# Optimization experiments

Measured on AMD Instinct MI355X. Metric: run time of the kernel, lower is better.

The kernel has to match this reference:

```python
import jax, jax.numpy as jnp
import numpy as np


def setup_inputs() -> dict:
    key = jax.random.key(0)
    k0, k1, k2, k3, k4 = jax.random.split(key, 5)
    B, S, D, H = 64, 512, 512, 512
    scale = 1.0 / np.sqrt(H)
    inp = {
        "input_features": jax.random.normal(k0, (B, S, D), dtype=jnp.float32),
        # PyTorch GRU params, gate order (r, z, n)
        "W_ih": jax.random.uniform(k1, (3 * H, D), jnp.float32, -scale, scale),
        "W_hh": jax.random.uniform(k2, (3 * H, H), jnp.float32, -scale, scale),
        "b_ih": jax.random.uniform(k3, (3 * H,), jnp.float32, -scale, scale),
        "b_hh": jax.random.uniform(k4, (3 * H,), jnp.float32, -scale, scale),
    }
    return inp


def reference(input_features, W_ih, W_hh, b_ih, b_hh):
    """1-layer unidirectional GRU with residual connection (input_dim == hidden_dim,
    so self.linear is Identity). Returns (residual_output [B,S,H],
    stacked per-step hidden [1,B,S,H]) matching the torch module."""
    B, S, D = input_features.shape
    H = W_hh.shape[1]

    # Precompute input projections for all timesteps in one GEMM: [B,S,3H]
    x_proj = jnp.einsum("bsd,gd->bsg", input_features, W_ih) + b_ih
    x_proj_t = jnp.transpose(x_proj, (1, 0, 2))  # [S,B,3H]

    def step(h, xp):
        # xp: [B,3H], h: [B,H]
        gh = h @ W_hh.T + b_hh  # [B,3H]
        r = jax.nn.sigmoid(xp[:, :H] + gh[:, :H])
        z = jax.nn.sigmoid(xp[:, H:2 * H] + gh[:, H:2 * H])
        n = jnp.tanh(xp[:, 2 * H:] + r * gh[:, 2 * H:])
        h_new = (1.0 - z) * n + z * h
        return h_new, h_new

    h0 = jnp.zeros((B, H), dtype=input_features.dtype)
    _, hs = jax.lax.scan(step, h0, x_proj_t)  # hs: [S,B,H]
    outputs = jnp.transpose(hs, (1, 0, 2))  # [B,S,H] raw GRU outputs

    residual_output = input_features + outputs  # Identity residual (D == H)
    hidden_stacked = outputs[None]  # [1,B,S,H]: per-step hidden of the single layer
    return residual_output, hidden_stacked
```

## Files before the change

### kernel.cpp

```cpp
#include <hip/hip_runtime.h>

typedef unsigned short u16;
typedef unsigned int   u32;
typedef unsigned long long u64;
typedef __attribute__((ext_vector_type(4))) float f32x4;
typedef __attribute__((ext_vector_type(8))) short s16x8;
typedef __attribute__((ext_vector_type(4))) unsigned short u16x4;
typedef __attribute__((ext_vector_type(8))) unsigned short u16x8;

__device__ __forceinline__ float bf2f(u16 u) {
    u32 i = ((u32)u) << 16;
    return __builtin_bit_cast(float, i);
}
__device__ __forceinline__ u16 f2bf(float f) {
    u32 i = __builtin_bit_cast(u32, f);
    u32 lsb = (i >> 16) & 1u;
    i += 0x7fffu + lsb;
    return (u16)(i >> 16);
}

__device__ __forceinline__ void ld_cc16(s16x8& r, const u16* p) {
    asm volatile("global_load_dwordx4 %0, %1, off sc0 sc1" : "=v"(r) : "v"(p));
}
__device__ __forceinline__ void st_cc8(u16* p, u64 v) {
    asm volatile("global_store_dwordx2 %0, %1, off sc0 sc1" :: "v"(p), "v"(v) : "memory");
}

__global__ __launch_bounds__(256) void prep(const float* __restrict__ Wih,
                                            const float* __restrict__ Whh,
                                            u16* __restrict__ Wihb,
                                            u16* __restrict__ Wfrag) {
    int id = blockIdx.x * 256 + threadIdx.x;
    {
        const float* s = Wih + (size_t)id * 8;
        f32x4 x0 = *(const f32x4*)s;
        f32x4 x1 = *(const f32x4*)(s + 4);
        u16x8 o;
        for (int j = 0; j < 4; ++j) { o[j] = f2bf(x0[j]); o[4 + j] = f2bf(x1[j]); }
        *(u16x8*)(Wihb + (size_t)id * 8) = o;
    }
    {
        int lane = id & 63;
        int ks   = (id >> 6) & 15;
        int wnt  = id >> 10;
        int nt   = wnt % 3;
        int w    = wnt / 3;
        int row  = nt * 512 + w * 16 + (lane & 15);
        int k    = ks * 32 + (lane >> 4) * 8;
        const float* s = Whh + (size_t)row * 512 + k;
        f32x4 x0 = *(const f32x4*)s;
        f32x4 x1 = *(const f32x4*)(s + 4);
        u16x8 o;
        for (int j = 0; j < 4; ++j) { o[j] = f2bf(x0[j]); o[4 + j] = f2bf(x1[j]); }
        *(u16x8*)(Wfrag + (size_t)id * 8) = o;
    }
}

__global__ __launch_bounds__(256) void gemm_xproj(const float* __restrict__ inp,
                                                  const u16* __restrict__ Wihb,
                                                  const float* __restrict__ bih,
                                                  u16* __restrict__ xp) {
    __shared__ u16 lA[128 * 64];
    __shared__ u16 lB[128 * 64];
    const int bid = blockIdx.x;
    const int mtile = bid & 255;
    const int ntile = bid >> 8;
    const int tid = threadIdx.x;
    const int l = tid & 63;
    const int wid = tid >> 6;
    const int s0 = mtile * 2;
    const int n0 = ntile * 128;

    f32x4 acc[4][4];
    for (int a = 0; a < 4; ++a)
        for (int b = 0; b < 4; ++b) acc[a][b] = (f32x4){0.f, 0.f, 0.f, 0.f};

    for (int k0 = 0; k0 < 512; k0 += 64) {
        if (k0) __syncthreads();
        for (int i = 0; i < 4; ++i) {
            int boff = (wid * 4 + i) * 1024 + l * 16;
            int r = boff >> 7;
            int kb = boff & 127;
            const char* src = (const char*)Wihb + (size_t)(n0 + r) * 1024 + (size_t)k0 * 2 + kb;
            __builtin_amdgcn_global_load_lds(
                (const __attribute__((address_space(1))) u32*)src,
                (__attribute__((address_space(3))) u32*)((char*)lB + (wid * 4 + i) * 1024),
                16, 0, 0);
        }
        for (int i = 0; i < 4; ++i) {
            int c = i * 256 + tid;
            int r = c >> 3;
            int ck = c & 7;
            int b = r & 63;
            int sl = r >> 6;
            const float* src = inp + ((size_t)(b * 512 + s0 + sl) * 512 + k0 + ck * 8);
            f32x4 x0 = *(const f32x4*)src;
            f32x4 x1 = *(const f32x4*)(src + 4);
            u16x8 o;
            for (int j = 0; j < 4; ++j) { o[j] = f2bf(x0[j]); o[4 + j] = f2bf(x1[j]); }
            *(u16x8*)(&lA[r * 64 + ck * 8]) = o;
        }
        __syncthreads();
        for (int kk = 0; kk < 2; ++kk) {
            s16x8 af[4], bf[4];
            for (int am = 0; am < 4; ++am)
                af[am] = *(const s16x8*)(&lA[((wid >> 1) * 64 + am * 16 + (l & 15)) * 64 + kk * 32 + (l >> 4) * 8]);
            for (int bn = 0; bn < 4; ++bn)
                bf[bn] = *(const s16x8*)(&lB[((wid & 1) * 64 + bn * 16 + (l & 15)) * 64 + kk * 32 + (l >> 4) * 8]);
            for (int am = 0; am < 4; ++am)
                for (int bn = 0; bn < 4; ++bn)
                    acc[am][bn] = __builtin_amdgcn_mfma_f32_16x16x32_bf16(af[am], bf[bn], acc[am][bn], 0, 0, 0);
        }
    }
    for (int am = 0; am < 4; ++am) {
        for (int bn = 0; bn < 4; ++bn) {
            int m_base = mtile * 128 + (wid >> 1) * 64 + am * 16;
            int row0 = m_base + ((l >> 4) << 2);
            int s = row0 >> 6;
            int b0 = row0 & 63;
            int n = n0 + (wid & 1) * 64 + bn * 16 + (l & 15);
            int g = n >> 9;
            int col = n & 511;
            int ww = col >> 4;
            int mt2 = b0 >> 4;
            size_t el = ((((size_t)s * 32 + ww) * 4 + mt2) * 3 + g) * 256 + l * 4;
            float bias = bih[n];
            u16x4 o;
            for (int j = 0; j < 4; ++j) o[j] = f2bf(acc[am][bn][j] + bias);
            *(u16x4*)(xp + el) = o;
        }
    }
}

__global__ __launch_bounds__(256, 1) void gru_scan(const u16* __restrict__ xp,
                                                   const u16* __restrict__ Wfrag,
                                                   const float* __restrict__ bhh,
                                                   const float* __restrict__ inp,
                                                   float* __restrict__ dout,
                                                   u16* __restrict__ hbuf,
                                                   int* __restrict__ cnt) {
    const int w = blockIdx.x;
    const int tid = threadIdx.x;
    const int l = tid & 63;
    const int mt = tid >> 6;
    float* out_res = dout;
    float* out_hid = dout + (size_t)64 * 512 * 512;

    __shared__ u16 tlds[4][16][20];

    const u16* wsrc = Wfrag + (size_t)w * 24576;
    s16x8 wreg[3][16];
#pragma unroll
    for (int g = 0; g < 3; ++g)
#pragma unroll
        for (int kk = 0; kk < 16; ++kk)
            wreg[g][kk] = *(const s16x8*)(wsrc + (size_t)(g * 16 + kk) * 512 + l * 8);

    const float bh0 = bhh[0 * 512 + w * 16 + (l & 15)];
    const float bh1 = bhh[1 * 512 + w * 16 + (l & 15)];
    const float bh2 = bhh[2 * 512 + w * 16 + (l & 15)];
    float hold[4] = {0.f, 0.f, 0.f, 0.f};
    const int bb = mt * 16 + ((l >> 4) << 2);
    const int c = w * 16 + (l & 15);

    s16x8 af[16];
#pragma unroll
    for (int kk = 0; kk < 16; ++kk) af[kk] = (s16x8){0, 0, 0, 0, 0, 0, 0, 0};

    const u16* xpp = xp + ((((size_t)0 * 32 + w) * 4 + mt) * 3) * 256 + l * 4;
    u16x4 xv0 = *(const u16x4*)(xpp);
    u16x4 xv1 = *(const u16x4*)(xpp + 256);
    u16x4 xv2 = *(const u16x4*)(xpp + 512);
    float inv[4];
#pragma unroll
    for (int j = 0; j < 4; ++j)
        inv[j] = inp[((size_t)(bb + j) * 512 + 0) * 512 + c];

    for (int t = 0; t < 512; ++t) {
        asm volatile("s_waitcnt vmcnt(0)" ::: "memory");
        __builtin_amdgcn_sched_barrier(0);

        f32x4 acc0 = (f32x4){0.f, 0.f, 0.f, 0.f};
        f32x4 acc1 = (f32x4){0.f, 0.f, 0.f, 0.f};
        f32x4 acc2 = (f32x4){0.f, 0.f, 0.f, 0.f};
#pragma unroll
        for (int kk = 0; kk < 16; ++kk) {
            acc0 = __builtin_amdgcn_mfma_f32_16x16x32_bf16(af[kk], wreg[0][kk], acc0, 0, 0, 0);
            acc1 = __builtin_amdgcn_mfma_f32_16x16x32_bf16(af[kk], wreg[1][kk], acc1, 0, 0, 0);
            acc2 = __builtin_amdgcn_mfma_f32_16x16x32_bf16(af[kk], wreg[2][kk], acc2, 0, 0, 0);
        }

        float hn[4];
#pragma unroll
        for (int j = 0; j < 4; ++j) {
            float xr = bf2f(xv0[j]), xz = bf2f(xv1[j]), xn = bf2f(xv2[j]);
            float rr = 1.f / (1.f + __expf(-(xr + acc0[j] + bh0)));
            float zz = 1.f / (1.f + __expf(-(xz + acc1[j] + bh1)));
            float nx = xn + rr * (acc2[j] + bh2);
            float e2 = __expf(-2.f * nx);
            float nn = (1.f - e2) / (1.f + e2);
            float h = (1.f - zz) * nn + zz * hold[j];
            hold[j] = h;
            hn[j] = h;
        }

        if (t < 511) {
#pragma unroll
            for (int j = 0; j < 4; ++j)
                tlds[mt][((l >> 4) << 2) + j][l & 15] = f2bf(hn[j]);
            u64 hv = *(const u64*)(&tlds[mt][l >> 2][(l & 3) * 4]);
            u16* hw = hbuf + (size_t)((t + 1) & 1) * 32768;
            st_cc8(hw + (size_t)(mt * 16 + (l >> 2)) * 512 + w * 16 + (l & 3) * 4, hv);
            asm volatile("s_waitcnt vmcnt(0)" ::: "memory");
            if (l == 0)
                __hip_atomic_fetch_add(&cnt[t], 1, __ATOMIC_RELAXED, __HIP_MEMORY_SCOPE_AGENT);
        }

#pragma unroll
        for (int j = 0; j < 4; ++j) {
            size_t oi = ((size_t)(bb + j) * 512 + t) * 512 + c;
            out_hid[oi] = hn[j];
            out_res[oi] = inv[j] + hn[j];
        }

        if (t < 511) {
            const u16* xq = xp + ((((size_t)(t + 1) * 32 + w) * 4 + mt) * 3) * 256 + l * 4;
            xv0 = *(const u16x4*)(xq);
            xv1 = *(const u16x4*)(xq + 256);
            xv2 = *(const u16x4*)(xq + 512);
#pragma unroll
            for (int j = 0; j < 4; ++j)
                inv[j] = inp[((size_t)(bb + j) * 512 + t + 1) * 512 + c];

            while (__hip_atomic_load(&cnt[t], __ATOMIC_RELAXED, __HIP_MEMORY_SCOPE_AGENT) < 128) {}
            __builtin_amdgcn_sched_barrier(0);

            const u16* hr = hbuf + (size_t)((t + 1) & 1) * 32768;
            const u16* hb = hr + (size_t)(mt * 16 + (l & 15)) * 512 + ((l >> 4) << 3);
#pragma unroll
            for (int kk = 0; kk < 16; ++kk)
                ld_cc16(af[kk], hb + kk * 32);
        }
    }
}

extern "C" void kernel_launch(void* const* d_in, const int* in_sizes, int n_in,
                              void* d_out, int out_size, void* d_ws, size_t ws_size,
                              hipStream_t stream) {
    const float* inp = (const float*)d_in[0];
    const float* Wih = (const float*)d_in[1];
    const float* Whh = (const float*)d_in[2];
    const float* bih = (const float*)d_in[3];
    const float* bhh = (const float*)d_in[4];
    float* out = (float*)d_out;

    char* ws = (char*)d_ws;
    int* cnt   = (int*)ws;
    u16* hbuf  = (u16*)(ws + 4096);
    u16* Wfrag = (u16*)(ws + 135168);
    u16* Wihb  = (u16*)(ws + 1708032);
    u16* xp    = (u16*)(ws + 3280896);

    hipMemsetAsync(ws, 0, 4096, stream);
    hipLaunchKernelGGL(prep, dim3(384), dim3(256), 0, stream, Wih, Whh, Wihb, Wfrag);
    hipLaunchKernelGGL(gemm_xproj, dim3(3072), dim3(256), 0, stream, inp, Wihb, bih, xp);
    hipLaunchKernelGGL(gru_scan, dim3(32), dim3(256), 0, stream, xp, Wfrag, bhh, inp, out, hbuf, cnt);
}
```

Baseline: 3.254 ms.

## Split hidden state into bf16 hi/lo pair and sync per batch tile

The recurrent hidden state is stored as a bf16 high part plus a bf16 residual low part. Both are multiplied by W_hh with separate MFMAs and summed, which recovers accuracy lost in plain bf16 rounding of h. This doubles the recurrent MFMA work and the hidden-state traffic per step. Synchronisation now uses a per-(batch tile, step) counter that waits on 32 arrivals instead of one global counter waiting on 128, so each wave only waits for its own batch rows. The gate math also switches to exp2/rcp intrinsics.

```diff
diff --git a/kernel.cpp b/kernel.cpp
--- a/kernel.cpp
+++ b/kernel.cpp
@@ -138,7 +138,7 @@
                                                    const float* __restrict__ inp,
                                                    float* __restrict__ dout,
                                                    u16* __restrict__ hbuf,
-                                                   int* __restrict__ cnt) {
+                                                   u32* __restrict__ cnt) {
     const int w = blockIdx.x;
     const int tid = threadIdx.x;
     const int l = tid & 63;
@@ -146,15 +146,21 @@
     float* out_res = dout;
     float* out_hid = dout + (size_t)64 * 512 * 512;
 
-    __shared__ u16 tlds[4][16][20];
-
-    const u16* wsrc = Wfrag + (size_t)w * 24576;
+    __shared__ u16 tldsh[4][16][20];
+    __shared__ u16 tldsl[4][16][20];
+
+    const volatile u32* wp = (const volatile u32*)(Wfrag + (size_t)w * 24576 + (size_t)l * 8);
     s16x8 wreg[3][16];
 #pragma unroll
     for (int g = 0; g < 3; ++g)
 #pragma unroll
-        for (int kk = 0; kk < 16; ++kk)
-            wreg[g][kk] = *(const s16x8*)(wsrc + (size_t)(g * 16 + kk) * 512 + l * 8);
+        for (int kk = 0; kk < 16; ++kk) {
+            int base = (g * 16 + kk) * 256;
+            union { u32 d[4]; s16x8 v; } uu;
+#pragma unroll
+            for (int q = 0; q < 4; ++q) uu.d[q] = wp[base + q];
+            wreg[g][kk] = uu.v;
+        }
 
     const float bh0 = bhh[0 * 512 + w * 16 + (l & 15)];
     const float bh1 = bhh[1 * 512 + w * 16 + (l & 15)];
@@ -163,9 +169,12 @@
     const int bb = mt * 16 + ((l >> 4) << 2);
     const int c = w * 16 + (l & 15);
 
-    s16x8 af[16];
-#pragma unroll
-    for (int kk = 0; kk < 16; ++kk) af[kk] = (s16x8){0, 0, 0, 0, 0, 0, 0, 0};
+    s16x8 afh[16], afl[16];
+#pragma unroll
+    for (int kk = 0; kk < 16; ++kk) {
+        afh[kk] = (s16x8){0, 0, 0, 0, 0, 0, 0, 0};
+        afl[kk] = (s16x8){0, 0, 0, 0, 0, 0, 0, 0};
+    }
 
     const u16* xpp = xp + ((((size_t)0 * 32 + w) * 4 + mt) * 3) * 256 + l * 4;
     u16x4 xv0 = *(const u16x4*)(xpp);
@@ -180,40 +189,59 @@
         asm volatile("s_waitcnt vmcnt(0)" ::: "memory");
         __builtin_amdgcn_sched_barrier(0);
 
-        f32x4 acc0 = (f32x4){0.f, 0.f, 0.f, 0.f};
-        f32x4 acc1 = (f32x4){0.f, 0.f, 0.f, 0.f};
-        f32x4 acc2 = (f32x4){0.f, 0.f, 0.f, 0.f};
+        f32x4 a0h = (f32x4){0.f,0.f,0.f,0.f}, a0l = (f32x4){0.f,0.f,0.f,0.f};
+        f32x4 a1h = (f32x4){0.f,0.f,0.f,0.f}, a1l = (f32x4){0.f,0.f,0.f,0.f};
+        f32x4 a2h = (f32x4){0.f,0.f,0.f,0.f}, a2l = (f32x4){0.f,0.f,0.f,0.f};
 #pragma unroll
         for (int kk = 0; kk < 16; ++kk) {
-            acc0 = __builtin_amdgcn_mfma_f32_16x16x32_bf16(af[kk], wreg[0][kk], acc0, 0, 0, 0);
-            acc1 = __builtin_amdgcn_mfma_f32_16x16x32_bf16(af[kk], wreg[1][kk], acc1, 0, 0, 0);
-            acc2 = __builtin_amdgcn_mfma_f32_16x16x32_bf16(af[kk], wreg[2][kk], acc2, 0, 0, 0);
+            a0h = __builtin_amdgcn_mfma_f32_16x16x32_bf16(afh[kk], wreg[0][kk], a0h, 0, 0, 0);
+            a1h = __builtin_amdgcn_mfma_f32_16x16x32_bf16(afh[kk], wreg[1][kk], a1h, 0, 0, 0);
+            a2h = __builtin_amdgcn_mfma_f32_16x16x32_bf16(afh[kk], wreg[2][kk], a2h, 0, 0, 0);
+            a0l = __builtin_amdgcn_mfma_f32_16x16x32_bf16(afl[kk], wreg[0][kk], a0l, 0, 0, 0);
+            a1l = __builtin_amdgcn_mfma_f32_16x16x32_bf16(afl[kk], wreg[1][kk], a1l, 0, 0, 0);
+            a2l = __builtin_amdgcn_mfma_f32_16x16x32_bf16(afl[kk], wreg[2][kk], a2l, 0, 0, 0);
         }
 
         float hn[4];
+        u16 hi16[4], lo16[4];
 #pragma unroll
         for (int j = 0; j < 4; ++j) {
+            float g0 = a0h[j] + a0l[j];
+            float g1 = a1h[j] + a1l[j];
+            float g2 = a2h[j] + a2l[j];
             float xr = bf2f(xv0[j]), xz = bf2f(xv1[j]), xn = bf2f(xv2[j]);
-            float rr = 1.f / (1.f + __expf(-(xr + acc0[j] + bh0)));
-            float zz = 1.f / (1.f + __expf(-(xz + acc1[j] + bh1)));
-            float nx = xn + rr * (acc2[j] + bh2);
-            float e2 = __expf(-2.f * nx);
-            float nn = (1.f - e2) / (1.f + e2);
-            float h = (1.f - zz) * nn + zz * hold[j];
+            float er = __builtin_amdgcn_exp2f(-1.44269504f * (xr + g0 + bh0));
+            float rr = __builtin_amdgcn_rcpf(1.f + er);
+            float ez = __builtin_amdgcn_exp2f(-1.44269504f * (xz + g1 + bh1));
+            float zz = __builtin_amdgcn_rcpf(1.f + ez);
+            float nx = xn + rr * (g2 + bh2);
+            float en = __builtin_amdgcn_exp2f(-2.88539008f * nx);
+            float nn = 2.f * __builtin_amdgcn_rcpf(1.f + en) - 1.f;
+            float h = zz * (hold[j] - nn) + nn;
             hold[j] = h;
             hn[j] = h;
-        }
-
+            u16 hi = f2bf(h);
+            float lo = h - bf2f(hi);
+            hi16[j] = hi;
+            lo16[j] = f2bf(lo);
+        }
+
+        const int ci = (mt * 512 + t) * 4;
         if (t < 511) {
 #pragma unroll
-            for (int j = 0; j < 4; ++j)
-                tlds[mt][((l >> 4) << 2) + j][l & 15] = f2bf(hn[j]);
-            u64 hv = *(const u64*)(&tlds[mt][l >> 2][(l & 3) * 4]);
-            u16* hw = hbuf + (size_t)((t + 1) & 1) * 32768;
-            st_cc8(hw + (size_t)(mt * 16 + (l >> 2)) * 512 + w * 16 + (l & 3) * 4, hv);
+            for (int j = 0; j < 4; ++j) {
+                tldsh[mt][((l >> 4) << 2) + j][l & 15] = hi16[j];
+                tldsl[mt][((l >> 4) << 2) + j][l & 15] = lo16[j];
+            }
+            u64 hvh = *(const u64*)(&tldsh[mt][l >> 2][(l & 3) * 4]);
+            u64 hvl = *(const u64*)(&tldsl[mt][l >> 2][(l & 3) * 4]);
+            u16* hw = hbuf + (size_t)((t + 1) & 1) * 65536;
+            size_t off = (size_t)(mt * 16 + (l >> 2)) * 512 + w * 16 + (l & 3) * 4;
+            st_cc8(hw + off, hvh);
+            st_cc8(hw + 32768 + off, hvl);
             asm volatile("s_waitcnt vmcnt(0)" ::: "memory");
             if (l == 0)
-                __hip_atomic_fetch_add(&cnt[t], 1, __ATOMIC_RELAXED, __HIP_MEMORY_SCOPE_AGENT);
+                __hip_atomic_fetch_add(&cnt[ci], 1, __ATOMIC_RELAXED, __HIP_MEMORY_SCOPE_AGENT);
         }
 
 #pragma unroll
@@ -232,14 +260,18 @@
             for (int j = 0; j < 4; ++j)
                 inv[j] = inp[((size_t)(bb + j) * 512 + t + 1) * 512 + c];
 
-            while (__hip_atomic_load(&cnt[t], __ATOMIC_RELAXED, __HIP_MEMORY_SCOPE_AGENT) < 128) {}
+            while (__hip_atomic_load(&cnt[ci], __ATOMIC_RELAXED,
+                                     __HIP_MEMORY_SCOPE_AGENT) < 32) {}
             __builtin_amdgcn_sched_barrier(0);
 
-            const u16* hr = hbuf + (size_t)((t + 1) & 1) * 32768;
+            const u16* hr = hbuf + (size_t)((t + 1) & 1) * 65536;
             const u16* hb = hr + (size_t)(mt * 16 + (l & 15)) * 512 + ((l >> 4) << 3);
 #pragma unroll
             for (int kk = 0; kk < 16; ++kk)
-                ld_cc16(af[kk], hb + kk * 32);
+                ld_cc16(afh[kk], hb + kk * 32);
+#pragma unroll
+            for (int kk = 0; kk < 16; ++kk)
+                ld_cc16(afl[kk], hb + 32768 + kk * 32);
         }
     }
 }
@@ -255,13 +287,13 @@
     float* out = (float*)d_out;
 
     char* ws = (char*)d_ws;
-    int* cnt   = (int*)ws;
-    u16* hbuf  = (u16*)(ws + 4096);
-    u16* Wfrag = (u16*)(ws + 135168);
-    u16* Wihb  = (u16*)(ws + 1708032);
-    u16* xp    = (u16*)(ws + 3280896);
-
-    hipMemsetAsync(ws, 0, 4096, stream);
+    u32* cnt   = (u32*)ws;
+    u16* hbuf  = (u16*)(ws + 32768);
+    u16* Wfrag = (u16*)(ws + 294912);
+    u16* Wihb  = (u16*)(ws + 1867776);
+    u16* xp    = (u16*)(ws + 3440640);
+
+    hipMemsetAsync(ws, 0, 32768, stream);
     hipLaunchKernelGGL(prep, dim3(384), dim3(256), 0, stream, Wih, Whh, Wihb, Wfrag);
     hipLaunchKernelGGL(gemm_xproj, dim3(3072), dim3(256), 0, stream, inp, Wihb, bih, xp);
     hipLaunchKernelGGL(gru_scan, dim3(32), dim3(256), 0, stream, xp, Wfrag, bhh, inp, out, hbuf, cnt);
```

After: 3.510 ms. +7.9%, slower.
